# Kernel tuning notes

Hardware: AMD Instinct MI355X
Metric: run time of the kernel (lower is better)

The kernel has to match this reference:

```python
import jax, jax.numpy as jnp
import numpy as np

NUM_NODES = 512
HEADS = 4
IN_F = 256
OUT_F = 128
EPS = 1e-5


def _layernorm(x, g, b):
    mu = jnp.mean(x, axis=-1, keepdims=True)
    var = jnp.mean(jnp.square(x - mu), axis=-1, keepdims=True)
    return (x - mu) * jax.lax.rsqrt(var + EPS) * g + b


def setup_inputs() -> dict:
    key = jax.random.key(0)
    ks = jax.random.split(key, 16)
    N = 32 * NUM_NODES
    E = 262144
    s = 0.05
    return {
        "x": jax.random.normal(ks[0], (N, IN_F), jnp.float32),
        "edge_index": jax.random.randint(ks[1], (2, E), 0, N, jnp.int64),
        "W_l": jax.random.normal(ks[2], (IN_F, HEADS * OUT_F), jnp.float32) * s,
        "W_r": jax.random.normal(ks[3], (IN_F, HEADS * OUT_F), jnp.float32) * s,
        "att": jax.random.normal(ks[4], (HEADS, OUT_F), jnp.float32) * s,
        "gat_bias": jnp.zeros((OUT_F,), jnp.float32),
        "gat_gamma": jnp.ones((OUT_F,), jnp.float32),
        "gat_beta": jnp.zeros((OUT_F,), jnp.float32),
        "cnn_W": jax.random.normal(ks[5], (IN_F, OUT_F), jnp.float32) * s,
        "cnn_b": jnp.zeros((OUT_F,), jnp.float32),
        "conv_W": jax.random.normal(ks[6], (OUT_F, OUT_F, 7), jnp.float32) * s,
        "conv_b": jnp.zeros((OUT_F,), jnp.float32),
        "cnn_gamma": jnp.ones((OUT_F,), jnp.float32),
        "cnn_beta": jnp.zeros((OUT_F,), jnp.float32),
        "res_W": jax.random.normal(ks[7], (IN_F, OUT_F), jnp.float32) * s,
        "res_b": jnp.zeros((OUT_F,), jnp.float32),
        "fuse_gamma": jnp.ones((OUT_F,), jnp.float32),
        "fuse_beta": jnp.zeros((OUT_F,), jnp.float32),
    }


def reference(x, edge_index, W_l, W_r, att, gat_bias, gat_gamma, gat_beta,
              cnn_W, cnn_b, conv_W, conv_b, cnn_gamma, cnn_beta,
              res_W, res_b, fuse_gamma, fuse_beta):
    N = x.shape[0]
    B = N // NUM_NODES
    # --- GATv2 branch (add self-loops like PyG default) ---
    loop = jnp.arange(N, dtype=edge_index.dtype)
    src = jnp.concatenate([edge_index[0], loop])
    dst = jnp.concatenate([edge_index[1], loop])
    x_l = (x @ W_l).reshape(N, HEADS, OUT_F)
    x_r = (x @ W_r).reshape(N, HEADS, OUT_F)
    e = x_l[src] + x_r[dst]                      # [E+N, H, F]
    e = jnp.where(e > 0, e, 0.2 * e)             # leaky_relu, slope 0.2
    score = jnp.einsum('ehf,hf->eh', e, att)     # [E+N, H]
    m = jax.ops.segment_max(score, dst, num_segments=N)
    ex = jnp.exp(score - m[dst])
    denom = jax.ops.segment_sum(ex, dst, num_segments=N)
    alpha = ex / denom[dst]
    agg = jax.ops.segment_sum(alpha[:, :, None] * x_l[src], dst, num_segments=N)
    h_gat = jnp.mean(agg, axis=1) + gat_bias     # concat=False -> head mean
    h_gat = jnp.where(h_gat > 0, h_gat, 0.01 * h_gat)  # nn.LeakyReLU default
    h_gat = _layernorm(h_gat, gat_gamma, gat_beta)
    # --- CNN branch ---
    xc = x @ cnn_W + cnn_b                       # [N, F]
    xc = xc.reshape(B, NUM_NODES, OUT_F).transpose(0, 2, 1)  # [B, F, L]
    hc = jax.lax.conv_general_dilated(xc, conv_W, window_strides=(1,),
                                      padding=[(3, 3)],
                                      dimension_numbers=('NCW', 'OIW', 'NCW'))
    hc = hc + conv_b[None, :, None]
    hc = hc.transpose(0, 2, 1).reshape(N, OUT_F)
    hc = jax.nn.relu(hc)
    hc = _layernorm(hc, cnn_gamma, cnn_beta)
    # --- fuse + residual ---
    h = h_gat + hc + (x @ res_W + res_b)
    return _layernorm(h, fuse_gamma, fuse_beta)
```

## Files before the change

kernel.cpp:

```cpp
#include <hip/hip_runtime.h>
#include <hip/hip_bf16.h>
#include <math.h>

#define IN_F 256
#define OUT_F 128
#define HEADS 4
#define HF 512
#define NCAT 1280

typedef __hip_bfloat16 bf16;
typedef unsigned short ushort_t;

using bf16x8 = __attribute__((ext_vector_type(8))) short;
using f32x4  = __attribute__((ext_vector_type(4))) float;

__device__ __forceinline__ float bflo(unsigned u) { return __uint_as_float(u << 16); }
__device__ __forceinline__ float bfhi(unsigned u) { return __uint_as_float(u & 0xffff0000u); }
__device__ __forceinline__ float bf2f(ushort_t u) { return __uint_as_float((unsigned)u << 16); }
__device__ __forceinline__ ushort_t f2bf(float f) {
    __hip_bfloat16 h = __float2bfloat16(f);
    return *reinterpret_cast<ushort_t*>(&h);
}

template <int CTRL>
__device__ __forceinline__ float dpp_add(float s) {
    int t = __builtin_amdgcn_update_dpp(0, __float_as_int(s), CTRL, 0xf, 0xf, true);
    return s + __int_as_float(t);
}
__device__ __forceinline__ float rowsum16(float s) {
    s = dpp_add<0x121>(s);
    s = dpp_add<0x122>(s);
    s = dpp_add<0x124>(s);
    s = dpp_add<0x128>(s);
    return s;
}

__global__ __launch_bounds__(256) void prep_kernel(
    const float* __restrict__ x, ushort_t* __restrict__ xb, int n_cvt,
    const float* __restrict__ Wl, const float* __restrict__ Wr,
    const float* __restrict__ Wc, const float* __restrict__ Wres,
    const float* __restrict__ Wconv,
    ushort_t* __restrict__ Wt, ushort_t* __restrict__ Wt2,
    const int* __restrict__ ei, int* __restrict__ counts, int E,
    int g1, int g2) {
    int b = blockIdx.x;
    if (b < g1) {
        int i = (b * 256 + threadIdx.x) * 8;
        if (i >= n_cvt) return;
        float4 a = *(const float4*)(x + i);
        float4 c = *(const float4*)(x + i + 4);
        uint4 o;
        o.x = f2bf(a.x) | ((unsigned)f2bf(a.y) << 16);
        o.y = f2bf(a.z) | ((unsigned)f2bf(a.w) << 16);
        o.z = f2bf(c.x) | ((unsigned)f2bf(c.y) << 16);
        o.w = f2bf(c.z) | ((unsigned)f2bf(c.w) << 16);
        *(uint4*)(xb + i) = o;
    } else if (b < g2) {
        int idx = (b - g1) * 256 + threadIdx.x;
        if (idx < NCAT * 256) {
            int n = idx >> 8, k = idx & 255;
            float v;
            if (n < 512)       v = Wl[(size_t)k * 512 + n];
            else if (n < 1024) v = Wr[(size_t)k * 512 + (n - 512)];
            else if (n < 1152) v = Wc[(size_t)k * 128 + (n - 1024)];
            else               v = Wres[(size_t)k * 128 + (n - 1152)];
            Wt[idx] = f2bf(v);
        } else {
            int j = idx - NCAT * 256;
            if (j < 7 * 128 * 128) {
                int k = j >> 14, o = (j >> 7) & 127, i = j & 127;
                Wt2[j] = f2bf(Wconv[((size_t)o * 128 + i) * 7 + k]);
            }
        }
    } else {
        int e = (b - g2) * 256 + threadIdx.x;
        if (e < E) atomicAdd(&counts[ei[E + e]], 1);
    }
}

__global__ __launch_bounds__(256) void mfma_gemm(
    const ushort_t* __restrict__ A,
    const ushort_t* __restrict__ Wt,
    ushort_t* __restrict__ xlb, ushort_t* __restrict__ xrb,
    ushort_t* __restrict__ xcb, ushort_t* __restrict__ resb,
    int M) {
    __shared__ ushort_t As[128][40];
    __shared__ ushort_t Bs[128][40];
    int tid = threadIdx.x;
    int lane = tid & 63, wid = tid >> 6;
    int wr = (wid >> 1) * 64, wc = (wid & 1) * 64;
    int brow = blockIdx.y * 128, bcol = blockIdx.x * 128;
    f32x4 acc[4][4] = {};
    int kb = (lane >> 4) * 8;
    int rl = lane & 15;
    for (int k0 = 0; k0 < 256; k0 += 32) {
        #pragma unroll
        for (int i = 0; i < 2; ++i) {
            int idx = tid + 256 * i;
            int row = idx >> 2, seg = idx & 3;
            *(uint4*)&As[row][seg * 8] =
                *(const uint4*)(A + (size_t)(brow + row) * 256 + k0 + seg * 8);
            *(uint4*)&Bs[row][seg * 8] =
                *(const uint4*)(Wt + (size_t)(bcol + row) * 256 + k0 + seg * 8);
        }
        __syncthreads();
        bf16x8 af[4], bfr[4];
        #pragma unroll
        for (int m = 0; m < 4; ++m) af[m] = *(const bf16x8*)&As[wr + m * 16 + rl][kb];
        #pragma unroll
        for (int n = 0; n < 4; ++n) bfr[n] = *(const bf16x8*)&Bs[wc + n * 16 + rl][kb];
        #pragma unroll
        for (int m = 0; m < 4; ++m)
            #pragma unroll
            for (int n = 0; n < 4; ++n)
                acc[m][n] = __builtin_amdgcn_mfma_f32_16x16x32_bf16(
                    af[m], bfr[n], acc[m][n], 0, 0, 0);
        __syncthreads();
    }
    ushort_t* dstp; int cstride, cb;
    if (bcol < 512)       { dstp = xlb;  cstride = 512; cb = bcol; }
    else if (bcol < 1024) { dstp = xrb;  cstride = 512; cb = bcol - 512; }
    else if (bcol < 1152) { dstp = xcb;  cstride = 128; cb = bcol - 1024; }
    else                  { dstp = resb; cstride = 128; cb = bcol - 1152; }
    int rowb = (lane >> 4) * 4;
    #pragma unroll
    for (int m = 0; m < 4; ++m)
        #pragma unroll
        for (int n = 0; n < 4; ++n) {
            int col = cb + wc + n * 16 + rl;
            #pragma unroll
            for (int q = 0; q < 4; ++q) {
                int row = brow + wr + m * 16 + rowb + q;
                dstp[(size_t)row * cstride + col] = f2bf(acc[m][n][q]);
            }
        }
}

__global__ __launch_bounds__(1024) void scan_kernel(
    const int* __restrict__ counts, int* __restrict__ offs,
    int* __restrict__ cursor, int N) {
    __shared__ int wsum[16];
    int t = threadIdx.x;
    int lane = t & 63, w = t >> 6;
    int base = t * 16;
    int local[16], s = 0;
    #pragma unroll
    for (int i = 0; i < 16; ++i) {
        int v = (base + i < N) ? counts[base + i] : 0;
        local[i] = v; s += v;
    }
    int sc = s;
    #pragma unroll
    for (int off = 1; off < 64; off <<= 1) {
        int v = __shfl_up(sc, off);
        if (lane >= off) sc += v;
    }
    if (lane == 63) wsum[w] = sc;
    __syncthreads();
    if (w == 0 && lane < 16) {
        int v = wsum[lane];
        int scv = v;
        #pragma unroll
        for (int off = 1; off < 16; off <<= 1) {
            int u = __shfl_up(scv, off);
            if (lane >= off) scv += u;
        }
        wsum[lane] = scv - v;
    }
    __syncthreads();
    int run = wsum[w] + sc - s;
    #pragma unroll
    for (int i = 0; i < 16; ++i) {
        if (base + i < N) { offs[base + i] = run; cursor[base + i] = run; }
        run += local[i];
    }
}

__global__ __launch_bounds__(256) void scatter_kernel(
    const int* __restrict__ ei, int* __restrict__ cursor,
    int* __restrict__ srcs, int E) {
    int e = blockIdx.x * 256 + threadIdx.x;
    if (e < E) {
        int d = ei[E + e];
        int p = atomicAdd(&cursor[d], 1);
        srcs[p] = ei[e];
    }
}

__global__ __launch_bounds__(256) void gat_fused_kernel(
    const ushort_t* __restrict__ xlb, const ushort_t* __restrict__ xrb,
    const int* __restrict__ srcs, const int* __restrict__ offs,
    const float* __restrict__ att, const float* __restrict__ gat_bias,
    const float* __restrict__ gat_gamma, const float* __restrict__ gat_beta,
    float* __restrict__ hgat_ln, int E, int N) {
    int wid = (blockIdx.x * 256 + threadIdx.x) >> 6;
    int lane = threadIdx.x & 63;
    if (wid >= N) return;
    int d = wid;
    const uint4 rv = ((const uint4*)(xrb + (size_t)d * HF))[lane];
    float xr8[8];
    xr8[0] = bflo(rv.x); xr8[1] = bfhi(rv.x);
    xr8[2] = bflo(rv.y); xr8[3] = bfhi(rv.y);
    xr8[4] = bflo(rv.z); xr8[5] = bfhi(rv.z);
    xr8[6] = bflo(rv.w); xr8[7] = bfhi(rv.w);
    const float4 a0 = ((const float4*)att)[lane * 2];
    const float4 a1 = ((const float4*)att)[lane * 2 + 1];
    const float aw[8] = {a0.x, a0.y, a0.z, a0.w, a1.x, a1.y, a1.z, a1.w};
    float acc[8] = {};
    float dn = 0.f;

    auto process = [&](uint4 lv) {
        float xl8[8];
        xl8[0] = bflo(lv.x); xl8[1] = bfhi(lv.x);
        xl8[2] = bflo(lv.y); xl8[3] = bfhi(lv.y);
        xl8[4] = bflo(lv.z); xl8[5] = bfhi(lv.z);
        xl8[6] = bflo(lv.w); xl8[7] = bfhi(lv.w);
        float s1 = 0.f, s2 = 0.f;
        #pragma unroll
        for (int j = 0; j < 8; ++j) {
            float v = xl8[j] + xr8[j];
            s1 = fmaf(v, aw[j], s1);
            s2 = fmaf(fabsf(v), aw[j], s2);
        }
        float s = fmaf(0.6f, s1, 0.4f * s2);
        s = rowsum16(s);
        float ex = __expf(s);
        dn += ex;
        #pragma unroll
        for (int j = 0; j < 8; ++j) acc[j] = fmaf(ex, xl8[j], acc[j]);
    };

    process(((const uint4*)(xlb + (size_t)d * HF))[lane]);

    int start = offs[d];
    int end = (d == N - 1) ? E : offs[d + 1];
    int p = start;
    for (; p + 3 < end; p += 4) {
        int s0 = srcs[p], s1 = srcs[p + 1], s2 = srcs[p + 2], s3 = srcs[p + 3];
        uint4 l0 = ((const uint4*)(xlb + (size_t)s0 * HF))[lane];
        uint4 l1 = ((const uint4*)(xlb + (size_t)s1 * HF))[lane];
        uint4 l2 = ((const uint4*)(xlb + (size_t)s2 * HF))[lane];
        uint4 l3 = ((const uint4*)(xlb + (size_t)s3 * HF))[lane];
        process(l0); process(l1); process(l2); process(l3);
    }
    for (; p < end; ++p)
        process(((const uint4*)(xlb + (size_t)srcs[p] * HF))[lane]);

    float inv = 1.f / dn;
    float v[8];
    #pragma unroll
    for (int j = 0; j < 8; ++j) {
        float t2 = acc[j] * inv;
        t2 += __shfl_xor(t2, 16);
        t2 += __shfl_xor(t2, 32);
        v[j] = t2;
    }
    int h = lane >> 4;
    int col = (lane & 15) * 8 + 2 * h;
    float g0 = 0.25f * v[2 * h]     + gat_bias[col];
    float g1 = 0.25f * v[2 * h + 1] + gat_bias[col + 1];
    g0 = g0 > 0.f ? g0 : 0.01f * g0;
    g1 = g1 > 0.f ? g1 : 0.01f * g1;
    float s = g0 + g1;
    #pragma unroll
    for (int off = 32; off; off >>= 1) s += __shfl_xor(s, off);
    float mu = s * (1.f / 128.f);
    float d0 = g0 - mu, d1 = g1 - mu;
    float vs = d0 * d0 + d1 * d1;
    #pragma unroll
    for (int off = 32; off; off >>= 1) vs += __shfl_xor(vs, off);
    float rinv = rsqrtf(vs * (1.f / 128.f) + 1e-5f);
    hgat_ln[(size_t)d * 128 + col]     = d0 * rinv * gat_gamma[col]     + gat_beta[col];
    hgat_ln[(size_t)d * 128 + col + 1] = d1 * rinv * gat_gamma[col + 1] + gat_beta[col + 1];
}

__global__ __launch_bounds__(256) void conv_fuse_kernel(
    const ushort_t* __restrict__ xcb, const float* __restrict__ cnn_b,
    const ushort_t* __restrict__ Wt2,
    const float* __restrict__ hgat_ln, const ushort_t* __restrict__ resb,
    const float* __restrict__ conv_b,
    const float* __restrict__ cnn_gamma, const float* __restrict__ cnn_beta,
    const float* __restrict__ res_b,
    const float* __restrict__ fuse_gamma, const float* __restrict__ fuse_beta,
    float* __restrict__ out) {
    __shared__ ushort_t As[38][136];
    __shared__ ushort_t Bs[128][136];
    __shared__ float hbuf[32][129];
    int tid = threadIdx.x;
    int lane = tid & 63, wid = tid >> 6;
    int wr = (wid >> 1) * 16, wc = (wid & 1) * 64;
    int b = blockIdx.y, l0 = blockIdx.x * 32;
    for (int u = tid; u < 38 * 16; u += 256) {
        int r = u >> 4, seg = u & 15;
        int l = l0 - 3 + r;
        uint4 o4 = make_uint4(0, 0, 0, 0);
        if (l >= 0 && l < 512) {
            uint4 v = *(const uint4*)(xcb + (size_t)(b * 512 + l) * 128 + seg * 8);
            float4 b0 = *(const float4*)(cnn_b + seg * 8);
            float4 b1 = *(const float4*)(cnn_b + seg * 8 + 4);
            o4.x = f2bf(bflo(v.x) + b0.x) | ((unsigned)f2bf(bfhi(v.x) + b0.y) << 16);
            o4.y = f2bf(bflo(v.y) + b0.z) | ((unsigned)f2bf(bfhi(v.y) + b0.w) << 16);
            o4.z = f2bf(bflo(v.z) + b1.x) | ((unsigned)f2bf(bfhi(v.z) + b1.y) << 16);
            o4.w = f2bf(bflo(v.w) + b1.z) | ((unsigned)f2bf(bfhi(v.w) + b1.w) << 16);
        }
        *(uint4*)&As[r][seg * 8] = o4;
    }
    f32x4 acc[4] = {};
    int rl = lane & 15, kb = (lane >> 4) * 8;
    for (int k = 0; k < 7; ++k) {
        __syncthreads();
        for (int u = tid; u < 128 * 16; u += 256) {
            int r = u >> 4, seg = u & 15;
            *(uint4*)&Bs[r][seg * 8] =
                *(const uint4*)(Wt2 + ((size_t)(k * 128 + r)) * 128 + seg * 8);
        }
        __syncthreads();
        #pragma unroll
        for (int kk = 0; kk < 4; ++kk) {
            bf16x8 af = *(const bf16x8*)&As[wr + rl + k][kk * 32 + kb];
            #pragma unroll
            for (int n = 0; n < 4; ++n) {
                bf16x8 bfr = *(const bf16x8*)&Bs[wc + n * 16 + rl][kk * 32 + kb];
                acc[n] = __builtin_amdgcn_mfma_f32_16x16x32_bf16(af, bfr, acc[n], 0, 0, 0);
            }
        }
    }
    __syncthreads();
    int rowb = (lane >> 4) * 4;
    #pragma unroll
    for (int n = 0; n < 4; ++n) {
        int col = wc + n * 16 + rl;
        float cb = conv_b[col];
        #pragma unroll
        for (int q = 0; q < 4; ++q) {
            int r = wr + rowb + q;
            hbuf[r][col] = fmaxf(acc[n][q] + cb, 0.f);
        }
    }
    __syncthreads();
    for (int r = wid * 8; r < wid * 8 + 8; ++r) {
        int grow = b * 512 + l0 + r;
        float h0 = hbuf[r][lane], h1 = hbuf[r][lane + 64];
        float s = h0 + h1;
        #pragma unroll
        for (int off = 32; off; off >>= 1) s += __shfl_xor(s, off);
        float mu = s * (1.f / 128.f);
        float d0 = h0 - mu, d1 = h1 - mu;
        float vs = d0 * d0 + d1 * d1;
        #pragma unroll
        for (int off = 32; off; off >>= 1) vs += __shfl_xor(vs, off);
        float inv = rsqrtf(vs * (1.f / 128.f) + 1e-5f);
        float hcn0 = d0 * inv * cnn_gamma[lane]      + cnn_beta[lane];
        float hcn1 = d1 * inv * cnn_gamma[lane + 64] + cnn_beta[lane + 64];
        size_t base = (size_t)grow * 128;
        float v0 = hgat_ln[base + lane]      + hcn0
                 + bf2f(resb[base + lane])      + res_b[lane];
        float v1 = hgat_ln[base + lane + 64] + hcn1
                 + bf2f(resb[base + lane + 64]) + res_b[lane + 64];
        s = v0 + v1;
        #pragma unroll
        for (int off = 32; off; off >>= 1) s += __shfl_xor(s, off);
        mu = s * (1.f / 128.f);
        d0 = v0 - mu; d1 = v1 - mu;
        vs = d0 * d0 + d1 * d1;
        #pragma unroll
        for (int off = 32; off; off >>= 1) vs += __shfl_xor(vs, off);
        inv = rsqrtf(vs * (1.f / 128.f) + 1e-5f);
        out[base + lane]      = d0 * inv * fuse_gamma[lane]      + fuse_beta[lane];
        out[base + lane + 64] = d1 * inv * fuse_gamma[lane + 64] + fuse_beta[lane + 64];
    }
}

extern "C" void kernel_launch(void* const* d_in, const int* in_sizes, int n_in,
                              void* d_out, int out_size, void* d_ws, size_t ws_size,
                              hipStream_t stream) {
    const float* x         = (const float*)d_in[0];
    const int*   ei        = (const int*)d_in[1];
    const float* W_l       = (const float*)d_in[2];
    const float* W_r       = (const float*)d_in[3];
    const float* att       = (const float*)d_in[4];
    const float* gat_bias  = (const float*)d_in[5];
    const float* gat_gamma = (const float*)d_in[6];
    const float* gat_beta  = (const float*)d_in[7];
    const float* cnn_W     = (const float*)d_in[8];
    const float* cnn_b     = (const float*)d_in[9];
    const float* conv_W    = (const float*)d_in[10];
    const float* conv_b    = (const float*)d_in[11];
    const float* cnn_gamma = (const float*)d_in[12];
    const float* cnn_beta  = (const float*)d_in[13];
    const float* res_W     = (const float*)d_in[14];
    const float* res_b     = (const float*)d_in[15];
    const float* fuse_gamma= (const float*)d_in[16];
    const float* fuse_beta = (const float*)d_in[17];

    int N = in_sizes[0] / IN_F;
    int E = in_sizes[1] / 2;

    char* ws = (char*)d_ws;
    size_t off = 0;
    ushort_t* xb     = (ushort_t*)(ws + off); off += (size_t)N * IN_F * 2;
    ushort_t* Wt     = (ushort_t*)(ws + off); off += (size_t)NCAT * IN_F * 2;
    ushort_t* Wt2    = (ushort_t*)(ws + off); off += (size_t)7 * 128 * 128 * 2;
    ushort_t* xlb    = (ushort_t*)(ws + off); off += (size_t)N * HF * 2;
    ushort_t* xrb    = (ushort_t*)(ws + off); off += (size_t)N * HF * 2;
    ushort_t* xcb    = (ushort_t*)(ws + off); off += (size_t)N * 128 * 2;
    ushort_t* resb   = (ushort_t*)(ws + off); off += (size_t)N * 128 * 2;
    int*  counts     = (int*)(ws + off);  off += (size_t)N * 4;
    int*  offs       = (int*)(ws + off);  off += (size_t)N * 4;
    int*  cursor     = (int*)(ws + off);  off += (size_t)N * 4;
    int*  srcs       = (int*)(ws + off);  off += (size_t)E * 4;
    float* hgat_ln   = (float*)(ws + off); off += (size_t)N * 128 * 4;

    hipMemsetAsync(counts, 0, (size_t)N * 4, stream);

    dim3 blk(256);
    int n_cvt = N * IN_F;
    int g1 = (n_cvt / 8 + 255) / 256;
    int g2 = g1 + (NCAT * 256 + 7 * 128 * 128 + 255) / 256;
    int g3 = g2 + (E + 255) / 256;
    prep_kernel<<<g3, blk, 0, stream>>>(x, xb, n_cvt,
        W_l, W_r, cnn_W, res_W, conv_W, Wt, Wt2, ei, counts, E, g1, g2);

    scan_kernel<<<1, 1024, 0, stream>>>(counts, offs, cursor, N);
    scatter_kernel<<<(E + 255) / 256, blk, 0, stream>>>(ei, cursor, srcs, E);

    mfma_gemm<<<dim3(NCAT / 128, N / 128), blk, 0, stream>>>(
        xb, Wt, xlb, xrb, xcb, resb, N);

    gat_fused_kernel<<<(N + 3) / 4, blk, 0, stream>>>(
        xlb, xrb, srcs, offs, att, gat_bias, gat_gamma, gat_beta, hgat_ln, E, N);

    conv_fuse_kernel<<<dim3(16, 32), blk, 0, stream>>>(
        xcb, cnn_b, Wt2, hgat_ln, resb, conv_b, cnn_gamma, cnn_beta,
        res_b, fuse_gamma, fuse_beta, (float*)d_out);
}
```

Measured before the change: 150.8 us.

## Use direct global-to-LDS loads with XOR swizzle in GEMM and conv kernels

Replaces register-staged global-to-shared copies in the projection GEMM and the conv weight tiles with global_load_lds direct-to-LDS transfers. The padded shared layouts become XOR-swizzled layouts to avoid bank conflicts. The GEMM K tile grows from 32 to 64, halving the number of barrier pairs. The GAT kernel also folds log2(e) into the attention weights and switches exp to exp2f. These changes aim to cut VGPR traffic, instruction count and synchronisation, at the cost of more intricate addressing and swizzle correctness risk.

```diff
diff --git a/kernel.cpp b/kernel.cpp
--- a/kernel.cpp
+++ b/kernel.cpp
@@ -20,6 +20,12 @@
 __device__ __forceinline__ ushort_t f2bf(float f) {
     __hip_bfloat16 h = __float2bfloat16(f);
     return *reinterpret_cast<ushort_t*>(&h);
+}
+
+__device__ __forceinline__ void gload16(const void* g, void* l) {
+    __builtin_amdgcn_global_load_lds(
+        (const __attribute__((address_space(1))) unsigned int*)g,
+        (__attribute__((address_space(3))) unsigned int*)l, 16, 0, 0);
 }
 
 template <int CTRL>
@@ -84,50 +90,61 @@
     ushort_t* __restrict__ xlb, ushort_t* __restrict__ xrb,
     ushort_t* __restrict__ xcb, ushort_t* __restrict__ resb,
     int M) {
-    __shared__ ushort_t As[128][40];
-    __shared__ ushort_t Bs[128][40];
+    __shared__ __align__(1024) ushort_t As[128 * 64];
+    __shared__ __align__(1024) ushort_t Bs[128 * 64];
     int tid = threadIdx.x;
     int lane = tid & 63, wid = tid >> 6;
     int wr = (wid >> 1) * 64, wc = (wid & 1) * 64;
     int brow = blockIdx.y * 128, bcol = blockIdx.x * 128;
+    int srow = lane >> 3;
+    int sslot = lane & 7;
+    int rl = lane & 15, kq = lane >> 4;
     f32x4 acc[4][4] = {};
-    int kb = (lane >> 4) * 8;
-    int rl = lane & 15;
-    for (int k0 = 0; k0 < 256; k0 += 32) {
-        #pragma unroll
-        for (int i = 0; i < 2; ++i) {
-            int idx = tid + 256 * i;
-            int row = idx >> 2, seg = idx & 3;
-            *(uint4*)&As[row][seg * 8] =
-                *(const uint4*)(A + (size_t)(brow + row) * 256 + k0 + seg * 8);
-            *(uint4*)&Bs[row][seg * 8] =
-                *(const uint4*)(Wt + (size_t)(bcol + row) * 256 + k0 + seg * 8);
+    for (int k0 = 0; k0 < 256; k0 += 64) {
+        #pragma unroll
+        for (int j = 0; j < 4; ++j) {
+            int r = (wid * 4 + j) * 8 + srow;
+            int sl = sslot ^ (r & 7);
+            gload16(A  + (size_t)(brow + r) * 256 + k0 + sl * 8,
+                    (char*)As + (wid * 4 + j) * 1024);
+            gload16(Wt + (size_t)(bcol + r) * 256 + k0 + sl * 8,
+                    (char*)Bs + (wid * 4 + j) * 1024);
         }
         __syncthreads();
-        bf16x8 af[4], bfr[4];
-        #pragma unroll
-        for (int m = 0; m < 4; ++m) af[m] = *(const bf16x8*)&As[wr + m * 16 + rl][kb];
-        #pragma unroll
-        for (int n = 0; n < 4; ++n) bfr[n] = *(const bf16x8*)&Bs[wc + n * 16 + rl][kb];
-        #pragma unroll
-        for (int m = 0; m < 4; ++m)
+        #pragma unroll
+        for (int ks = 0; ks < 2; ++ks) {
+            int cb = ks * 64 + kq * 16;
+            bf16x8 af[4], bfv[4];
             #pragma unroll
-            for (int n = 0; n < 4; ++n)
-                acc[m][n] = __builtin_amdgcn_mfma_f32_16x16x32_bf16(
-                    af[m], bfr[n], acc[m][n], 0, 0, 0);
+            for (int m = 0; m < 4; ++m) {
+                int r = wr + m * 16 + rl;
+                af[m] = *(const bf16x8*)((const char*)As + r * 128 + (cb ^ ((r & 7) << 4)));
+            }
+            #pragma unroll
+            for (int n = 0; n < 4; ++n) {
+                int r = wc + n * 16 + rl;
+                bfv[n] = *(const bf16x8*)((const char*)Bs + r * 128 + (cb ^ ((r & 7) << 4)));
+            }
+            #pragma unroll
+            for (int m = 0; m < 4; ++m)
+                #pragma unroll
+                for (int n = 0; n < 4; ++n)
+                    acc[m][n] = __builtin_amdgcn_mfma_f32_16x16x32_bf16(
+                        af[m], bfv[n], acc[m][n], 0, 0, 0);
+        }
         __syncthreads();
     }
-    ushort_t* dstp; int cstride, cb;
-    if (bcol < 512)       { dstp = xlb;  cstride = 512; cb = bcol; }
-    else if (bcol < 1024) { dstp = xrb;  cstride = 512; cb = bcol - 512; }
-    else if (bcol < 1152) { dstp = xcb;  cstride = 128; cb = bcol - 1024; }
-    else                  { dstp = resb; cstride = 128; cb = bcol - 1152; }
+    ushort_t* dstp; int cstride, cb2;
+    if (bcol < 512)       { dstp = xlb;  cstride = 512; cb2 = bcol; }
+    else if (bcol < 1024) { dstp = xrb;  cstride = 512; cb2 = bcol - 512; }
+    else if (bcol < 1152) { dstp = xcb;  cstride = 128; cb2 = bcol - 1024; }
+    else                  { dstp = resb; cstride = 128; cb2 = bcol - 1152; }
     int rowb = (lane >> 4) * 4;
     #pragma unroll
     for (int m = 0; m < 4; ++m)
         #pragma unroll
         for (int n = 0; n < 4; ++n) {
-            int col = cb + wc + n * 16 + rl;
+            int col = cb2 + wc + n * 16 + rl;
             #pragma unroll
             for (int q = 0; q < 4; ++q) {
                 int row = brow + wr + m * 16 + rowb + q;
@@ -203,9 +220,11 @@
     xr8[2] = bflo(rv.y); xr8[3] = bfhi(rv.y);
     xr8[4] = bflo(rv.z); xr8[5] = bfhi(rv.z);
     xr8[6] = bflo(rv.w); xr8[7] = bfhi(rv.w);
+    const float LOG2E = 1.44269504f;
     const float4 a0 = ((const float4*)att)[lane * 2];
     const float4 a1 = ((const float4*)att)[lane * 2 + 1];
-    const float aw[8] = {a0.x, a0.y, a0.z, a0.w, a1.x, a1.y, a1.z, a1.w};
+    const float aw[8] = {a0.x * LOG2E, a0.y * LOG2E, a0.z * LOG2E, a0.w * LOG2E,
+                         a1.x * LOG2E, a1.y * LOG2E, a1.z * LOG2E, a1.w * LOG2E};
     float acc[8] = {};
     float dn = 0.f;
 
@@ -224,7 +243,7 @@
         }
         float s = fmaf(0.6f, s1, 0.4f * s2);
         s = rowsum16(s);
-        float ex = __expf(s);
+        float ex = exp2f(s);
         dn += ex;
         #pragma unroll
         for (int j = 0; j < 8; ++j) acc[j] = fmaf(ex, xl8[j], acc[j]);
@@ -284,7 +303,7 @@
     const float* __restrict__ fuse_gamma, const float* __restrict__ fuse_beta,
     float* __restrict__ out) {
     __shared__ ushort_t As[38][136];
-    __shared__ ushort_t Bs[128][136];
+    __shared__ __align__(1024) ushort_t Bs[128 * 128];
     __shared__ float hbuf[32][129];
     int tid = threadIdx.x;
     int lane = tid & 63, wid = tid >> 6;
@@ -307,20 +326,26 @@
     }
     f32x4 acc[4] = {};
     int rl = lane & 15, kb = (lane >> 4) * 8;
+    int sr4 = lane >> 4, ss = lane & 15;
     for (int k = 0; k < 7; ++k) {
         __syncthreads();
-        for (int u = tid; u < 128 * 16; u += 256) {
-            int r = u >> 4, seg = u & 15;
-            *(uint4*)&Bs[r][seg * 8] =
-                *(const uint4*)(Wt2 + ((size_t)(k * 128 + r)) * 128 + seg * 8);
+        #pragma unroll
+        for (int j = 0; j < 8; ++j) {
+            int r = (wid * 8 + j) * 4 + sr4;
+            int sl = ss ^ (r & 15);
+            gload16(Wt2 + ((size_t)(k * 128 + r)) * 128 + sl * 8,
+                    (char*)Bs + (wid * 8 + j) * 1024);
         }
         __syncthreads();
         #pragma unroll
         for (int kk = 0; kk < 4; ++kk) {
             bf16x8 af = *(const bf16x8*)&As[wr + rl + k][kk * 32 + kb];
+            int cbyte = kk * 64 + (lane >> 4) * 16;
             #pragma unroll
             for (int n = 0; n < 4; ++n) {
-                bf16x8 bfr = *(const bf16x8*)&Bs[wc + n * 16 + rl][kk * 32 + kb];
+                int r = wc + n * 16 + rl;
+                bf16x8 bfr = *(const bf16x8*)((const char*)Bs + r * 256
+                                              + (cbyte ^ ((r & 15) << 4)));
                 acc[n] = __builtin_amdgcn_mfma_f32_16x16x32_bf16(af, bfr, acc[n], 0, 0, 0);
             }
         }
```

Result: faster. 144.1 us (-4.4%).
